# Kernel optimization log

Measured on AMD Instinct MI355X. Metric: run time of the kernel, lower is better.

The kernel has to match this reference:

```python
import jax, jax.numpy as jnp
import numpy as np

DIM = 1152
HEADS = 9
MID = 256
B, N = 8, 1024


def _conprefix(x, dw, db, uw, ub):
    # torch Linear: y = x @ W.T + b
    kv = jnp.tanh(x @ dw.T + db) @ uw.T + ub  # [B, N, 2*dim]
    q = jnp.zeros(kv.shape[:2] + (DIM,), kv.dtype)
    return jnp.concatenate([q, kv], axis=-1)  # [B, N, 3*dim]


def setup_inputs() -> dict:
    key = jax.random.key(0)
    ks = jax.random.split(key, 12)
    s = 0.02
    return {
        "x": jax.random.normal(ks[0], (B, N, DIM), dtype=jnp.float32),
        "Wqkv": jax.random.normal(ks[1], (3 * DIM, DIM), dtype=jnp.float32) * s,
        "Wproj": jax.random.normal(ks[2], (DIM, DIM), dtype=jnp.float32) * s,
        "bproj": jax.random.normal(ks[3], (DIM,), dtype=jnp.float32) * s,
        "down_w": jax.random.normal(ks[4], (MID, DIM), dtype=jnp.float32) * s,
        "down_b": jax.random.normal(ks[5], (MID,), dtype=jnp.float32) * s,
        "up_w": jax.random.normal(ks[6], (2 * DIM, MID), dtype=jnp.float32) * s,
        "up_b": jax.random.normal(ks[7], (2 * DIM,), dtype=jnp.float32) * s,
        "pdown_w": jax.random.normal(ks[8], (MID, DIM), dtype=jnp.float32) * s,
        "pdown_b": jax.random.normal(ks[9], (MID,), dtype=jnp.float32) * s,
        "pup_w": jax.random.normal(ks[10], (2 * DIM, MID), dtype=jnp.float32) * s,
        "pup_b": jax.random.normal(ks[11], (2 * DIM,), dtype=jnp.float32) * s,
        "task": 5,
    }


def reference(x, Wqkv, Wproj, bproj, down_w, down_b, up_w, up_b,
              pdown_w, pdown_b, pup_w, pup_b, task):
    b, n, c = x.shape
    hd = c // HEADS
    scale = hd ** (-0.5)
    qkv = x @ Wqkv.T  # [B, N, 3C] (qkv_bias=False)
    task_prefix_tensor = None
    if task <= 3:
        pass
    elif task == 4:
        qkv = qkv + _conprefix(x, down_w, down_b, up_w, up_b)
        task_prefix_tensor = down_w
    else:
        qkv = (qkv + _conprefix(x, pdown_w, pdown_b, pup_w, pup_b)
                   + _conprefix(x, down_w, down_b, up_w, up_b))
        task_prefix_tensor = down_w
    qkv = qkv.reshape(b, n, 3, HEADS, hd).transpose(2, 0, 3, 1, 4)  # [3,B,H,N,hd]
    q, k, v = qkv[0], qkv[1], qkv[2]
    attn = jax.nn.softmax(jnp.einsum('bhqd,bhkd->bhqk', q, k) * scale, axis=-1)
    out = jnp.einsum('bhqk,bhkd->bhqd', attn, v)  # [B,H,N,hd]
    out = out.transpose(0, 2, 1, 3).reshape(b, n, c)
    out = out @ Wproj.T + bproj
    return (out, task_prefix_tensor)
```

## Files before the change

### kernel.cpp

```cpp
#include <hip/hip_runtime.h>
#include <math.h>

namespace {

typedef unsigned short u16;
typedef __attribute__((ext_vector_type(8))) short short8;
typedef __attribute__((ext_vector_type(4))) float f32x4;
typedef __attribute__((ext_vector_type(16))) float f32x16;

constexpr int kDim   = 1152;
constexpr int kHeads = 9;
constexpr int kMid   = 256;
constexpr int kB     = 8;
constexpr int kN     = 1024;
constexpr int kM     = kB * kN;
constexpr int kQS    = 3584;
constexpr float kCexp  = 0.12753837360881433f;

__device__ __forceinline__ u16 f2bf(float f) {
    unsigned u = __builtin_bit_cast(unsigned, f);
    return (u16)((u + 0x7FFFu + ((u >> 16) & 1u)) >> 16);
}
__device__ __forceinline__ float bf2f(u16 h) {
    unsigned u = ((unsigned)h) << 16;
    return __builtin_bit_cast(float, u);
}

__device__ __forceinline__ void gload_lds16(const void* g, void* l) {
    __builtin_amdgcn_global_load_lds(
        (const __attribute__((address_space(1))) unsigned int*)g,
        (__attribute__((address_space(3))) unsigned int*)l,
        16, 0, 0);
}

__device__ __forceinline__ unsigned cvtpk(float a, float b) {
    unsigned r;
    asm volatile("v_cvt_pk_bf16_f32 %0, %1, %2" : "=v"(r) : "v"(a), "v"(b));
    return r;
}

__device__ __forceinline__ void halfswap(unsigned& x, unsigned& y, bool hihalf) {
    const unsigned xs = (unsigned)__shfl_xor((int)x, 32);
    const unsigned ys = (unsigned)__shfl_xor((int)y, 32);
    const unsigned nx = hihalf ? ys : x;
    const unsigned ny = hihalf ? y : xs;
    x = nx; y = ny;
}

__device__ __forceinline__ short8 build_pfrag(float p0, float p1, float p2, float p3,
                                              float p4, float p5, float p6, float p7,
                                              bool hihalf) {
    unsigned x1 = cvtpk(p0, p1), y1 = cvtpk(p4, p5);
    unsigned x2 = cvtpk(p2, p3), y2 = cvtpk(p6, p7);
    halfswap(x1, y1, hihalf);
    halfswap(x2, y2, hihalf);
    union { unsigned u[4]; short8 s; } pk;
    pk.u[0] = x1; pk.u[1] = x2; pk.u[2] = y1; pk.u[3] = y2;
    return pk.s;
}

constexpr int R0 = 2359296;
constexpr int R1 = R0 + 995328;
constexpr int R2 = R1 + 331776;
constexpr int R3 = R2 + 73728;
constexpr int R4 = R3 + 73728;
constexpr int R5 = R4 + 147456;
constexpr int R6 = R5 + 147456;
constexpr int R7 = R6 + 512;
constexpr int R8 = R7 + 2304;
constexpr int kQPart = 331776;
constexpr int kPrepGrid = R8 / 256;

__global__ __launch_bounds__(256)
void prep_all(const float* __restrict__ x, const float* __restrict__ Wqkv,
              const float* __restrict__ Wproj,
              const float* __restrict__ down_w, const float* __restrict__ pdown_w,
              const float* __restrict__ up_w, const float* __restrict__ pup_w,
              const float* __restrict__ down_b, const float* __restrict__ pdown_b,
              const float* __restrict__ up_b, const float* __restrict__ pup_b,
              const int* __restrict__ task,
              u16* __restrict__ xb, u16* __restrict__ wqkvb, u16* __restrict__ wprjb,
              u16* __restrict__ wdownb, u16* __restrict__ wupb,
              float* __restrict__ bd, float* __restrict__ bu)
{
    const int i = blockIdx.x * blockDim.x + threadIdx.x;
    auto cvt4s = [](const float* s, int j, float sc) {
        const float4 v = reinterpret_cast<const float4*>(s)[j];
        ushort4 o;
        o.x = f2bf(v.x * sc); o.y = f2bf(v.y * sc);
        o.z = f2bf(v.z * sc); o.w = f2bf(v.w * sc);
        return o;
    };
    if (i < R0) {
        reinterpret_cast<ushort4*>(xb)[i] = cvt4s(x, i, 1.f);
    } else if (i < R1) {
        const int j = i - R0;
        const float sc = (j < kQPart) ? kCexp : 1.f;
        reinterpret_cast<ushort4*>(wqkvb)[j] = cvt4s(Wqkv, j, sc);
    } else if (i < R2) {
        reinterpret_cast<ushort4*>(wprjb)[i - R1] = cvt4s(Wproj, i - R1, 1.f);
    } else if (i < R3) {
        reinterpret_cast<ushort4*>(wdownb)[i - R2] = cvt4s(down_w, i - R2, 1.f);
    } else if (i < R4) {
        reinterpret_cast<ushort4*>(wdownb)[73728 + (i - R3)] = cvt4s(pdown_w, i - R3, 1.f);
    } else if (i < R5) {
        const int j = i - R4, r = j >> 6, c = j & 63;
        reinterpret_cast<ushort4*>(wupb)[r * 128 + c] = cvt4s(up_w, j, 1.f);
    } else if (i < R6) {
        const int j = i - R5, r = j >> 6, c = j & 63;
        reinterpret_cast<ushort4*>(wupb)[r * 128 + 64 + c] = cvt4s(pup_w, j, 1.f);
    } else if (i < R7) {
        const int j = i - R6;
        bd[j] = (j < 256) ? down_b[j] : pdown_b[j - 256];
    } else {
        const int j = i - R7;
        bu[j] = up_b[j] + ((*task >= 5) ? pup_b[j] : 0.f);
    }
}

template<bool ACCUM, bool BIAS>
__global__ __launch_bounds__(512, 2)
void gemm8p(const u16* __restrict__ A, const u16* __restrict__ Bw,
            const float* __restrict__ bias, u16* __restrict__ C,
            int K, int lda, int ldb, int ldc)
{
    extern __shared__ char lds[];

    const int tid  = threadIdx.x;
    const int lane = tid & 63;
    const int wid  = tid >> 6;
    const int wm   = wid >> 2;
    const int wn   = wid & 3;
    const int bm   = blockIdx.x * 256;
    const int bn   = blockIdx.y * 256;
    const int l15  = lane & 15;
    const int kq   = lane >> 4;

    int srow[4], scol[4], sdst[4];
#pragma unroll
    for (int i = 0; i < 4; ++i) {
        const int id = i * 512 + tid;
        srow[i] = id >> 3;
        const int s = id & 7;
        scol[i] = (s ^ (srow[i] & 7)) * 8;
        sdst[i] = (i * 512 + wid * 64) * 16;
    }

    auto stage_pair = [&](int buf, int kt, int i) {
        const u16* ag = A  + (size_t)bm * lda + kt * 64;
        const u16* bg = Bw + (size_t)bn * ldb + kt * 64;
        gload_lds16(ag + (size_t)srow[i] * lda + scol[i], lds + buf * 32768 + sdst[i]);
        gload_lds16(bg + (size_t)srow[i] * ldb + scol[i], lds + 65536 + buf * 32768 + sdst[i]);
    };

    f32x4 acc[8][4] = {};
    const int nt = K >> 6;

#pragma unroll
    for (int i = 0; i < 4; ++i) stage_pair(0, 0, i);

    for (int t = 0; t < nt; ++t) {
        const char* Ab = lds + (t & 1) * 32768;
        const char* Bb = lds + 65536 + (t & 1) * 32768;
        const bool nxt = (t + 1 < nt);
        const int nb = (t + 1) & 1;

        short8 af[4], bf[4];

        auto rdA = [&](int mh, int ks) {
#pragma unroll
            for (int mi = 0; mi < 4; ++mi) {
                const int row = wm * 128 + mh * 64 + mi * 16 + l15;
                af[mi] = *reinterpret_cast<const short8*>(
                    Ab + row * 128 + (((ks * 4 + kq) ^ (row & 7)) * 16));
            }
        };
        auto rdB = [&](int ks) {
#pragma unroll
            for (int ni = 0; ni < 4; ++ni) {
                const int row = wn * 64 + ni * 16 + l15;
                bf[ni] = *reinterpret_cast<const short8*>(
                    Bb + row * 128 + (((ks * 4 + kq) ^ (row & 7)) * 16));
            }
        };
        auto mfma16 = [&](int mh) {
            asm volatile("s_waitcnt lgkmcnt(0)" ::: "memory");
            __builtin_amdgcn_sched_barrier(0);
            __builtin_amdgcn_s_setprio(1);
#pragma unroll
            for (int mi = 0; mi < 4; ++mi)
#pragma unroll
                for (int ni = 0; ni < 4; ++ni)
                    acc[mh * 4 + mi][ni] = __builtin_amdgcn_mfma_f32_16x16x32_bf16(
                        af[mi], bf[ni], acc[mh * 4 + mi][ni], 0, 0, 0);
            __builtin_amdgcn_s_setprio(0);
            asm volatile("" ::: "memory");
            __builtin_amdgcn_s_barrier();
            asm volatile("" ::: "memory");
        };

        if (nxt) { stage_pair(nb, t + 1, 0); stage_pair(nb, t + 1, 1); }
        if (nxt) asm volatile("s_waitcnt vmcnt(4)" ::: "memory");
        else     asm volatile("s_waitcnt vmcnt(0)" ::: "memory");
        __builtin_amdgcn_sched_barrier(0);
        __builtin_amdgcn_s_barrier();
        asm volatile("" ::: "memory");
        rdB(0); rdA(0, 0);
        mfma16(0);

        if (nxt) { stage_pair(nb, t + 1, 2); stage_pair(nb, t + 1, 3); }
        rdA(1, 0);
        mfma16(1);

        rdB(1); rdA(0, 1);
        mfma16(0);

        rdA(1, 1);
        mfma16(1);
    }

#pragma unroll
    for (int mg = 0; mg < 8; ++mg) {
#pragma unroll
        for (int ni = 0; ni < 4; ++ni) {
            const int col = bn + wn * 64 + ni * 16 + l15;
            const float bv = BIAS ? bias[col] : 0.f;
#pragma unroll
            for (int r = 0; r < 4; ++r) {
                const int row = bm + wm * 128 + mg * 16 + kq * 4 + r;
                float v = acc[mg][ni][r] + bv;
                u16* cp = C + (size_t)row * ldc + col;
                if (ACCUM) v += bf2f(*cp);
                *cp = f2bf(v);
            }
        }
    }
}

template<bool TANH, bool ACCUM, bool BIAS, bool OUT_BF16, bool KSEL>
__global__ __launch_bounds__(256)
void gemm_mfma(const u16* __restrict__ A, const u16* __restrict__ Bw,
               const float* __restrict__ bias, void* __restrict__ Cv,
               int K, int lda, int ldb, int ldc,
               const int* __restrict__ taskp, int mintask)
{
    if (taskp != nullptr && *taskp < mintask) return;
    if (KSEL && *taskp < 5) K = 256;

    __shared__ u16 As[2][128 * 64];
    __shared__ u16 Bs[2][128 * 64];

    const int tid  = threadIdx.x;
    const int lane = tid & 63;
    const int wv   = tid >> 6;
    const int wr   = (wv >> 1) * 64;
    const int wc   = (wv & 1) * 64;
    const int bm   = blockIdx.x * 128;
    const int bn   = blockIdx.y * 128;

    f32x4 acc[4][4] = {};

    const int srow = tid >> 3;
    const int sslt = tid & 7;

    auto stage = [&](int buf, int k0) {
        const u16* ab = A  + (size_t)bm * lda + k0;
        const u16* bb = Bw + (size_t)bn * ldb + k0;
#pragma unroll
        for (int i = 0; i < 4; ++i) {
            const int row = i * 32 + srow;
            gload_lds16(ab + (size_t)row * lda + sslt * 8,
                        (char*)&As[buf][0] + (i * 256 + (tid & 192)) * 16);
        }
#pragma unroll
        for (int i = 0; i < 4; ++i) {
            const int row = i * 32 + srow;
            gload_lds16(bb + (size_t)row * ldb + sslt * 8,
                        (char*)&Bs[buf][0] + (i * 256 + (tid & 192)) * 16);
        }
    };

    stage(0, 0);
    const int nk = K >> 6;
    for (int kt = 0; kt < nk; ++kt) {
        __syncthreads();
        if (kt + 1 < nk) stage((kt + 1) & 1, (kt + 1) * 64);
        const u16* as = &As[kt & 1][0];
        const u16* bs = &Bs[kt & 1][0];
#pragma unroll
        for (int ks = 0; ks < 2; ++ks) {
            short8 af[4], bf[4];
#pragma unroll
            for (int mi = 0; mi < 4; ++mi) {
                const int row = wr + mi * 16 + (lane & 15);
                af[mi] = *reinterpret_cast<const short8*>(as + row * 64 + ks * 32 + (lane >> 4) * 8);
            }
#pragma unroll
            for (int ni = 0; ni < 4; ++ni) {
                const int row = wc + ni * 16 + (lane & 15);
                bf[ni] = *reinterpret_cast<const short8*>(bs + row * 64 + ks * 32 + (lane >> 4) * 8);
            }
#pragma unroll
            for (int mi = 0; mi < 4; ++mi)
#pragma unroll
                for (int ni = 0; ni < 4; ++ni)
                    acc[mi][ni] = __builtin_amdgcn_mfma_f32_16x16x32_bf16(
                        af[mi], bf[ni], acc[mi][ni], 0, 0, 0);
        }
    }

#pragma unroll
    for (int mi = 0; mi < 4; ++mi) {
#pragma unroll
        for (int ni = 0; ni < 4; ++ni) {
            const int col = bn + wc + ni * 16 + (lane & 15);
            const float bv = BIAS ? bias[col] : 0.f;
#pragma unroll
            for (int r = 0; r < 4; ++r) {
                const int row = bm + wr + mi * 16 + (lane >> 4) * 4 + r;
                float v = acc[mi][ni][r] + bv;
                if (TANH) v = tanhf(v);
                if (OUT_BF16) {
                    u16* cp = (u16*)Cv + (size_t)row * ldc + col;
                    if (ACCUM) v += bf2f(*cp);
                    *cp = f2bf(v);
                } else {
                    float* cp = (float*)Cv + (size_t)row * ldc + col;
                    if (ACCUM) v += *cp;
                    *cp = v;
                }
            }
        }
    }
}

__global__ __launch_bounds__(256)
void transpose_v(const u16* __restrict__ qkv, u16* __restrict__ vt)
{
    __shared__ u16 t[64][136];
    const int bh = blockIdx.x, b = bh / kHeads, h = bh - b * kHeads;
    const int n0 = blockIdx.y * 64;
    const int tid = threadIdx.x;
#pragma unroll
    for (int it = 0; it < 4; ++it) {
        const int I = it * 256 + tid, tok = I >> 4, s = I & 15;
        *reinterpret_cast<short8*>(&t[tok][s * 8]) =
            *reinterpret_cast<const short8*>(
                qkv + (size_t)(b * kN + n0 + tok) * kQS + 2304 + h * 128 + s * 8);
    }
    __syncthreads();
#pragma unroll
    for (int it = 0; it < 8; ++it) {
        const int I = it * 256 + tid;
        const int d = I >> 4, tk = (I & 15) * 4;
        ushort4 v;
        v.x = t[tk + 0][d]; v.y = t[tk + 1][d];
        v.z = t[tk + 2][d]; v.w = t[tk + 3][d];
        *reinterpret_cast<ushort4*>(vt + (size_t)(bh * 128 + d) * kN + n0 + tk) = v;
    }
}

__global__ __launch_bounds__(256)
void attn_mfma(const u16* __restrict__ qkv, const u16* __restrict__ vt,
               u16* __restrict__ out)
{
    __shared__ u16 Ks[2][32 * 128];
    __shared__ u16 Vs[2][128 * 32];

    const int bh = blockIdx.x, b = bh / kHeads, h = bh - b * kHeads;
    const int tid = threadIdx.x, lane = tid & 63, wv = tid >> 6;
    const int lo5 = lane & 31;
    const bool hihalf = (lane >= 32);
    const int hi = hihalf ? 1 : 0;
    const int qh = wv >> 1;
    const int kh = wv & 1;
    const int q0 = blockIdx.y * 64 + qh * 32;

    const u16* qp = qkv + (size_t)(b * kN + q0 + lo5) * kQS + h * 128;
    short8 qf[8];
#pragma unroll
    for (int f = 0; f < 8; ++f)
        qf[f] = *reinterpret_cast<const short8*>(qp + f * 16 + hi * 8);

    int koff[2], voff[2];
#pragma unroll
    for (int j = 0; j < 2; ++j) {
        const int I = j * 256 + tid;
        const int tok = I >> 4, s = I & 15;
        koff[j] = tok * kQS + ((s ^ (tok & 7)) * 8);
        const int d = I >> 2, sv = I & 3;
        voff[j] = d * kN + ((sv ^ (d & 3)) * 8);
    }
    const u16* kbase = qkv + (size_t)b * kN * kQS + kDim + h * 128;
    const u16* vbase = vt + (size_t)bh * 128 * kN;

    f32x16 o[4] = {};
    float l = 0.f;

    for (int t = 0; t < 16; ++t) {
        __syncthreads();
#pragma unroll
        for (int hh = 0; hh < 2; ++hh) {
            const int kt = hh * 512 + t * 32;
#pragma unroll
            for (int j = 0; j < 2; ++j) {
                gload_lds16(kbase + (size_t)kt * kQS + koff[j],
                            (char*)&Ks[hh][0] + (j * 256 + wv * 64) * 16);
                gload_lds16(vbase + kt + voff[j],
                            (char*)&Vs[hh][0] + (j * 256 + wv * 64) * 16);
            }
        }
        __syncthreads();

        const char* ks = (const char*)&Ks[kh][0];
        const char* vs = (const char*)&Vs[kh][0];

        f32x16 s0 = {};
        __builtin_amdgcn_s_setprio(1);
#pragma unroll
        for (int f = 0; f < 8; ++f) {
            const short8 ka = *reinterpret_cast<const short8*>(
                ks + lo5 * 256 + (((f * 2 + hi) * 16) ^ ((lo5 & 7) << 4)));
            s0 = __builtin_amdgcn_mfma_f32_32x32x16_bf16(ka, qf[f], s0, 0, 0, 0);
        }
        __builtin_amdgcn_s_setprio(0);

        float rsum = 0.f;
#pragma unroll
        for (int r = 0; r < 16; ++r) { s0[r] = exp2f(s0[r]); rsum += s0[r]; }
        rsum += __shfl_xor(rsum, 32);
        l += rsum;

        short8 pf[2];
        pf[0] = build_pfrag(s0[0], s0[1], s0[2], s0[3], s0[4], s0[5], s0[6], s0[7], hihalf);
        pf[1] = build_pfrag(s0[8], s0[9], s0[10], s0[11], s0[12], s0[13], s0[14], s0[15], hihalf);

        __builtin_amdgcn_s_setprio(1);
#pragma unroll
        for (int dt = 0; dt < 4; ++dt) {
            const int drow = dt * 32 + lo5;
#pragma unroll
            for (int c = 0; c < 2; ++c) {
                const short8 va = *reinterpret_cast<const short8*>(
                    vs + drow * 64 + (((c * 2 + hi) * 16) ^ ((drow & 3) << 4)));
                o[dt] = __builtin_amdgcn_mfma_f32_32x32x16_bf16(va, pf[c], o[dt], 0, 0, 0);
            }
        }
        __builtin_amdgcn_s_setprio(0);
    }

    __syncthreads();
    char* exch = (char*)&Ks[0][0];
    float* ls  = (float*)&Vs[0][0];
    if (kh == 1) {
#pragma unroll
        for (int dt = 0; dt < 4; ++dt) {
#pragma unroll
            for (int rg = 0; rg < 4; ++rg) {
                const int kb = (dt * 4 + rg) * 8;
                ushort4 w;
                w.x = f2bf(o[dt][rg * 4 + 0]);
                w.y = f2bf(o[dt][rg * 4 + 1]);
                w.z = f2bf(o[dt][rg * 4 + 2]);
                w.w = f2bf(o[dt][rg * 4 + 3]);
                *reinterpret_cast<ushort4*>(
                    exch + qh * 8192 + lane * 128 + (kb ^ ((lane & 7) << 3))) = w;
            }
        }
        if (!hihalf) ls[qh * 32 + lo5] = l;
    }
    __syncthreads();
    if (kh == 0) {
        const float inv = 1.f / (l + ls[qh * 32 + lo5]);
        u16* op = out + (size_t)(b * kN + q0 + lo5) * kDim + h * 128;
#pragma unroll
        for (int dt = 0; dt < 4; ++dt) {
#pragma unroll
            for (int rg = 0; rg < 4; ++rg) {
                const int kb = (dt * 4 + rg) * 8;
                const ushort4 pv = *reinterpret_cast<const ushort4*>(
                    exch + qh * 8192 + lane * 128 + (kb ^ ((lane & 7) << 3)));
                const int d0 = dt * 32 + rg * 8 + hi * 4;
                ushort4 v;
                v.x = f2bf((o[dt][rg * 4 + 0] + bf2f(pv.x)) * inv);
                v.y = f2bf((o[dt][rg * 4 + 1] + bf2f(pv.y)) * inv);
                v.z = f2bf((o[dt][rg * 4 + 2] + bf2f(pv.z)) * inv);
                v.w = f2bf((o[dt][rg * 4 + 3] + bf2f(pv.w)) * inv);
                *reinterpret_cast<ushort4*>(op + d0) = v;
            }
        }
    }
}

}

extern "C" void kernel_launch(void* const* d_in, const int* in_sizes, int n_in,
                              void* d_out, int out_size, void* d_ws, size_t ws_size,
                              hipStream_t stream)
{
    const float* x       = (const float*)d_in[0];
    const float* Wqkv    = (const float*)d_in[1];
    const float* Wproj   = (const float*)d_in[2];
    const float* bproj   = (const float*)d_in[3];
    const float* down_w  = (const float*)d_in[4];
    const float* down_b  = (const float*)d_in[5];
    const float* up_w    = (const float*)d_in[6];
    const float* up_b    = (const float*)d_in[7];
    const float* pdown_w = (const float*)d_in[8];
    const float* pdown_b = (const float*)d_in[9];
    const float* pup_w   = (const float*)d_in[10];
    const float* pup_b   = (const float*)d_in[11];
    const int*   task    = (const int*)d_in[12];

    u16* xb_vt  = (u16*)d_ws;
    u16* wqkvb  = xb_vt  + (size_t)kM * kDim;
    u16* wprjb  = wqkvb  + (size_t)kQS * kDim;
    u16* wdownb = wprjb  + (size_t)kDim * kDim;
    u16* wupb   = wdownb + (size_t)512 * kDim;
    u16* h12    = wupb   + (size_t)2304 * 512;
    u16* qkvb   = h12    + (size_t)kM * 512;
    u16* aob    = qkvb   + (size_t)kM * kQS;
    float* bd   = (float*)(aob + (size_t)kM * kDim);
    float* bu   = bd + 512;
    float* out  = (float*)d_out;
    u16* xb = xb_vt;
    u16* vt = xb_vt;

    prep_all<<<kPrepGrid, 256, 0, stream>>>(
        x, Wqkv, Wproj, down_w, pdown_w, up_w, pup_w,
        down_b, pdown_b, up_b, pup_b, task,
        xb, wqkvb, wprjb, wdownb, wupb, bd, bu);

    hipFuncSetAttribute(reinterpret_cast<const void*>(&gemm8p<false, false>),
                        hipFuncAttributeMaxDynamicSharedMemorySize, 131072);

    gemm_mfma<true, false, true, true, false><<<dim3(kM / 128, 4), 256, 0, stream>>>(
        xb, wdownb, bd, h12, kDim, kDim, kDim, 512, nullptr, 0);
    gemm8p<false, false><<<dim3(kM / 256, kQS / 256), 512, 131072, stream>>>(
        xb, wqkvb, nullptr, qkvb, kDim, kDim, kDim, kQS);
    gemm_mfma<false, true, true, true, true><<<dim3(kM / 128, 18), 256, 0, stream>>>(
        h12, wupb, bu, qkvb + kDim, 512, 512, 512, kQS, task, 4);

    transpose_v<<<dim3(kB * kHeads, kN / 64), 256, 0, stream>>>(qkvb, vt);

    attn_mfma<<<dim3(kB * kHeads, kN / 64), 256, 0, stream>>>(qkvb, vt, aob);

    gemm_mfma<false, false, true, false, false><<<dim3(kM / 128, 9), 256, 0, stream>>>(
        aob, wprjb, bproj, out, kDim, kDim, kDim, kDim, nullptr, 0);

    hipMemcpyAsync(out + (size_t)kM * kDim, down_w,
                   (size_t)kMid * kDim * sizeof(float),
                   hipMemcpyDeviceToDevice, stream);
}
```

Baseline: 330.4 us.

## Halve GEMM K-tile to cut LDS use; restage attention K/V tiles

The QKV GEMM kernel drops its K-step from 64 to 32. That halves dynamic LDS from 128KB to 64KB, and the launch bounds now ask for 4 blocks per CU instead of 2, trading twice as many barriers and stages for higher occupancy. The attention kernel now loads one 64-row K tile and a 128x64 V tile per iteration into single unified LDS buffers with 8-way XOR swizzles, in place of two separate 32-wide halves. That changes the load mapping and the bank-conflict pattern. The request for 4 blocks of 512 threads may force register spilling given the 128 accumulator floats per thread.

```diff
diff --git a/kernel.cpp b/kernel.cpp
--- a/kernel.cpp
+++ b/kernel.cpp
@@ -119,8 +119,8 @@
 }
 
 template<bool ACCUM, bool BIAS>
-__global__ __launch_bounds__(512, 2)
-void gemm8p(const u16* __restrict__ A, const u16* __restrict__ Bw,
+__global__ __launch_bounds__(512, 4)
+void gemm2b(const u16* __restrict__ A, const u16* __restrict__ Bw,
             const float* __restrict__ bias, u16* __restrict__ C,
             int K, int lda, int ldb, int ldc)
 {
@@ -136,51 +136,50 @@
     const int l15  = lane & 15;
     const int kq   = lane >> 4;
 
-    int srow[4], scol[4], sdst[4];
-#pragma unroll
-    for (int i = 0; i < 4; ++i) {
+    int srow[2], scol[2], sdst[2];
+#pragma unroll
+    for (int i = 0; i < 2; ++i) {
         const int id = i * 512 + tid;
-        srow[i] = id >> 3;
-        const int s = id & 7;
-        scol[i] = (s ^ (srow[i] & 7)) * 8;
+        srow[i] = id >> 2;
+        const int s = id & 3;
+        scol[i] = (s ^ (srow[i] & 3)) * 8;
         sdst[i] = (i * 512 + wid * 64) * 16;
     }
 
-    auto stage_pair = [&](int buf, int kt, int i) {
-        const u16* ag = A  + (size_t)bm * lda + kt * 64;
-        const u16* bg = Bw + (size_t)bn * ldb + kt * 64;
-        gload_lds16(ag + (size_t)srow[i] * lda + scol[i], lds + buf * 32768 + sdst[i]);
-        gload_lds16(bg + (size_t)srow[i] * ldb + scol[i], lds + 65536 + buf * 32768 + sdst[i]);
+    auto stage = [&](int buf, int kt) {
+        const u16* ag = A  + (size_t)bm * lda + kt * 32;
+        const u16* bg = Bw + (size_t)bn * ldb + kt * 32;
+#pragma unroll
+        for (int i = 0; i < 2; ++i) {
+            gload_lds16(ag + (size_t)srow[i] * lda + scol[i], lds + buf * 16384 + sdst[i]);
+            gload_lds16(bg + (size_t)srow[i] * ldb + scol[i], lds + 32768 + buf * 16384 + sdst[i]);
+        }
     };
 
     f32x4 acc[8][4] = {};
-    const int nt = K >> 6;
-
-#pragma unroll
-    for (int i = 0; i < 4; ++i) stage_pair(0, 0, i);
+    const int nt = K >> 5;
+
+    stage(0, 0);
 
     for (int t = 0; t < nt; ++t) {
-        const char* Ab = lds + (t & 1) * 32768;
-        const char* Bb = lds + 65536 + (t & 1) * 32768;
+        const char* Ab = lds + (t & 1) * 16384;
+        const char* Bb = lds + 32768 + (t & 1) * 16384;
         const bool nxt = (t + 1 < nt);
-        const int nb = (t + 1) & 1;
+
+        if (nxt) stage((t + 1) & 1, t + 1);
+        if (nxt) asm volatile("s_waitcnt vmcnt(4)" ::: "memory");
+        else     asm volatile("s_waitcnt vmcnt(0)" ::: "memory");
+        __builtin_amdgcn_sched_barrier(0);
+        __builtin_amdgcn_s_barrier();
+        asm volatile("" ::: "memory");
 
         short8 af[4], bf[4];
-
-        auto rdA = [&](int mh, int ks) {
+        auto rdA = [&](int mh) {
 #pragma unroll
             for (int mi = 0; mi < 4; ++mi) {
                 const int row = wm * 128 + mh * 64 + mi * 16 + l15;
                 af[mi] = *reinterpret_cast<const short8*>(
-                    Ab + row * 128 + (((ks * 4 + kq) ^ (row & 7)) * 16));
-            }
-        };
-        auto rdB = [&](int ks) {
-#pragma unroll
-            for (int ni = 0; ni < 4; ++ni) {
-                const int row = wn * 64 + ni * 16 + l15;
-                bf[ni] = *reinterpret_cast<const short8*>(
-                    Bb + row * 128 + (((ks * 4 + kq) ^ (row & 7)) * 16));
+                    Ab + row * 64 + ((kq ^ (row & 3)) * 16));
             }
         };
         auto mfma16 = [&](int mh) {
@@ -199,23 +198,15 @@
             asm volatile("" ::: "memory");
         };
 
-        if (nxt) { stage_pair(nb, t + 1, 0); stage_pair(nb, t + 1, 1); }
-        if (nxt) asm volatile("s_waitcnt vmcnt(4)" ::: "memory");
-        else     asm volatile("s_waitcnt vmcnt(0)" ::: "memory");
-        __builtin_amdgcn_sched_barrier(0);
-        __builtin_amdgcn_s_barrier();
-        asm volatile("" ::: "memory");
-        rdB(0); rdA(0, 0);
+#pragma unroll
+        for (int ni = 0; ni < 4; ++ni) {
+            const int row = wn * 64 + ni * 16 + l15;
+            bf[ni] = *reinterpret_cast<const short8*>(
+                Bb + row * 64 + ((kq ^ (row & 3)) * 16));
+        }
+        rdA(0);
         mfma16(0);
-
-        if (nxt) { stage_pair(nb, t + 1, 2); stage_pair(nb, t + 1, 3); }
-        rdA(1, 0);
-        mfma16(1);
-
-        rdB(1); rdA(0, 1);
-        mfma16(0);
-
-        rdA(1, 1);
+        rdA(1);
         mfma16(1);
     }
 
@@ -364,8 +355,8 @@
 void attn_mfma(const u16* __restrict__ qkv, const u16* __restrict__ vt,
                u16* __restrict__ out)
 {
-    __shared__ u16 Ks[2][32 * 128];
-    __shared__ u16 Vs[2][128 * 32];
+    __shared__ u16 Ks[64 * 128];
+    __shared__ u16 Vs[128 * 64];
 
     const int bh = blockIdx.x, b = bh / kHeads, h = bh - b * kHeads;
     const int tid = threadIdx.x, lane = tid & 63, wv = tid >> 6;
@@ -382,14 +373,16 @@
     for (int f = 0; f < 8; ++f)
         qf[f] = *reinterpret_cast<const short8*>(qp + f * 16 + hi * 8);
 
-    int koff[2], voff[2];
-#pragma unroll
-    for (int j = 0; j < 2; ++j) {
+    int koff[4], voff[4];
+#pragma unroll
+    for (int j = 0; j < 4; ++j) {
         const int I = j * 256 + tid;
-        const int tok = I >> 4, s = I & 15;
-        koff[j] = tok * kQS + ((s ^ (tok & 7)) * 8);
-        const int d = I >> 2, sv = I & 3;
-        voff[j] = d * kN + ((sv ^ (d & 3)) * 8);
+        const int row = I >> 4, s = I & 15;
+        const int tokK = (row >> 5) * 512 + (row & 31);
+        koff[j] = tokK * kQS + ((s ^ (row & 7)) * 8);
+        const int d = I >> 3, u = I & 7;
+        const int cs = u ^ (d & 7);
+        voff[j] = d * kN + ((cs >> 2) * 512 + (cs & 3) * 8);
     }
     const u16* kbase = qkv + (size_t)b * kN * kQS + kDim + h * 128;
     const u16* vbase = vt + (size_t)bh * 128 * kN;
@@ -400,27 +393,22 @@
     for (int t = 0; t < 16; ++t) {
         __syncthreads();
 #pragma unroll
-        for (int hh = 0; hh < 2; ++hh) {
-            const int kt = hh * 512 + t * 32;
-#pragma unroll
-            for (int j = 0; j < 2; ++j) {
-                gload_lds16(kbase + (size_t)kt * kQS + koff[j],
-                            (char*)&Ks[hh][0] + (j * 256 + wv * 64) * 16);
-                gload_lds16(vbase + kt + voff[j],
-                            (char*)&Vs[hh][0] + (j * 256 + wv * 64) * 16);
-            }
-        }
+        for (int j = 0; j < 4; ++j)
+            gload_lds16(kbase + (size_t)(t * 32) * kQS + koff[j],
+                        (char*)Ks + (j * 256 + wv * 64) * 16);
+#pragma unroll
+        for (int j = 0; j < 4; ++j)
+            gload_lds16(vbase + t * 32 + voff[j],
+                        (char*)Vs + (j * 256 + wv * 64) * 16);
         __syncthreads();
 
-        const char* ks = (const char*)&Ks[kh][0];
-        const char* vs = (const char*)&Vs[kh][0];
-
+        const int rr = kh * 32 + lo5;
         f32x16 s0 = {};
         __builtin_amdgcn_s_setprio(1);
 #pragma unroll
         for (int f = 0; f < 8; ++f) {
             const short8 ka = *reinterpret_cast<const short8*>(
-                ks + lo5 * 256 + (((f * 2 + hi) * 16) ^ ((lo5 & 7) << 4)));
+                (const char*)Ks + rr * 256 + (((f * 2 + hi) * 16) ^ ((rr & 7) << 4)));
             s0 = __builtin_amdgcn_mfma_f32_32x32x16_bf16(ka, qf[f], s0, 0, 0, 0);
         }
         __builtin_amdgcn_s_setprio(0);
@@ -442,7 +430,8 @@
 #pragma unroll
             for (int c = 0; c < 2; ++c) {
                 const short8 va = *reinterpret_cast<const short8*>(
-                    vs + drow * 64 + (((c * 2 + hi) * 16) ^ ((drow & 3) << 4)));
+                    (const char*)Vs + drow * 128 +
+                    (((kh * 4 + c * 2 + hi) * 16) ^ ((drow & 7) << 4)));
                 o[dt] = __builtin_amdgcn_mfma_f32_32x32x16_bf16(va, pf[c], o[dt], 0, 0, 0);
             }
         }
@@ -450,8 +439,8 @@
     }
 
     __syncthreads();
-    char* exch = (char*)&Ks[0][0];
-    float* ls  = (float*)&Vs[0][0];
+    char* exch = (char*)Ks;
+    float* ls  = (float*)Vs;
     if (kh == 1) {
 #pragma unroll
         for (int dt = 0; dt < 4; ++dt) {
@@ -531,12 +520,12 @@
         down_b, pdown_b, up_b, pup_b, task,
         xb, wqkvb, wprjb, wdownb, wupb, bd, bu);
 
-    hipFuncSetAttribute(reinterpret_cast<const void*>(&gemm8p<false, false>),
-                        hipFuncAttributeMaxDynamicSharedMemorySize, 131072);
+    hipFuncSetAttribute(reinterpret_cast<const void*>(&gemm2b<false, false>),
+                        hipFuncAttributeMaxDynamicSharedMemorySize, 65536);
 
     gemm_mfma<true, false, true, true, false><<<dim3(kM / 128, 4), 256, 0, stream>>>(
         xb, wdownb, bd, h12, kDim, kDim, kDim, 512, nullptr, 0);
-    gemm8p<false, false><<<dim3(kM / 256, kQS / 256), 512, 131072, stream>>>(
+    gemm2b<false, false><<<dim3(kM / 256, kQS / 256), 512, 65536, stream>>>(
         xb, wqkvb, nullptr, qkvb, kDim, kDim, kDim, kQS);
     gemm_mfma<false, true, true, true, true><<<dim3(kM / 128, 18), 256, 0, stream>>>(
         h12, wupb, bu, qkvb + kDim, 512, 512, 512, kQS, task, 4);
```

Result: slower. 719.9 us (+117.9%).

## Fuse V transpose into up-projection epilogue and register-prefetch K/V tiles in attention

Applied to the files above, without the earlier changes.

Removes the standalone transpose_v kernel by having the prefix up-projection GEMM epilogue write the V columns directly into the transposed vt buffer. When the task gate is off, the kernel still runs with a zero gate so that vt is produced. The attention kernel replaces direct global-to-LDS loads with a register-staged prefetch of the next K/V tile, overlapping global loads with MFMA compute. The trade-offs are extra register pressure and strided 8-byte stores in the GEMM epilogue.

```diff
diff --git a/kernel.cpp b/kernel.cpp
--- a/kernel.cpp
+++ b/kernel.cpp
@@ -237,14 +237,19 @@
     }
 }
 
-template<bool TANH, bool ACCUM, bool BIAS, bool OUT_BF16, bool KSEL>
+template<bool TANH, bool ACCUM, bool BIAS, bool OUT_BF16, bool KSEL, bool VT>
 __global__ __launch_bounds__(256)
 void gemm_mfma(const u16* __restrict__ A, const u16* __restrict__ Bw,
                const float* __restrict__ bias, void* __restrict__ Cv,
+               u16* __restrict__ vt,
                int K, int lda, int ldb, int ldc,
                const int* __restrict__ taskp, int mintask)
 {
-    if (taskp != nullptr && *taskp < mintask) return;
+    float gate = 1.f;
+    if (taskp != nullptr && *taskp < mintask) {
+        if (!VT) return;
+        gate = 0.f;
+    }
     if (KSEL && *taskp < 5) K = 256;
 
     __shared__ u16 As[2][128 * 64];
@@ -315,48 +320,34 @@
         for (int ni = 0; ni < 4; ++ni) {
             const int col = bn + wc + ni * 16 + (lane & 15);
             const float bv = BIAS ? bias[col] : 0.f;
+            ushort4 tv;
 #pragma unroll
             for (int r = 0; r < 4; ++r) {
                 const int row = bm + wr + mi * 16 + (lane >> 4) * 4 + r;
-                float v = acc[mi][ni][r] + bv;
+                float v = gate * (acc[mi][ni][r] + bv);
                 if (TANH) v = tanhf(v);
                 if (OUT_BF16) {
                     u16* cp = (u16*)Cv + (size_t)row * ldc + col;
                     if (ACCUM) v += bf2f(*cp);
-                    *cp = f2bf(v);
+                    const u16 bb = f2bf(v);
+                    *cp = bb;
+                    if (VT) (&tv.x)[r] = bb;
                 } else {
                     float* cp = (float*)Cv + (size_t)row * ldc + col;
                     if (ACCUM) v += *cp;
                     *cp = v;
                 }
             }
-        }
-    }
-}
-
-__global__ __launch_bounds__(256)
-void transpose_v(const u16* __restrict__ qkv, u16* __restrict__ vt)
-{
-    __shared__ u16 t[64][136];
-    const int bh = blockIdx.x, b = bh / kHeads, h = bh - b * kHeads;
-    const int n0 = blockIdx.y * 64;
-    const int tid = threadIdx.x;
-#pragma unroll
-    for (int it = 0; it < 4; ++it) {
-        const int I = it * 256 + tid, tok = I >> 4, s = I & 15;
-        *reinterpret_cast<short8*>(&t[tok][s * 8]) =
-            *reinterpret_cast<const short8*>(
-                qkv + (size_t)(b * kN + n0 + tok) * kQS + 2304 + h * 128 + s * 8);
-    }
-    __syncthreads();
-#pragma unroll
-    for (int it = 0; it < 8; ++it) {
-        const int I = it * 256 + tid;
-        const int d = I >> 4, tk = (I & 15) * 4;
-        ushort4 v;
-        v.x = t[tk + 0][d]; v.y = t[tk + 1][d];
-        v.z = t[tk + 2][d]; v.w = t[tk + 3][d];
-        *reinterpret_cast<ushort4*>(vt + (size_t)(bh * 128 + d) * kN + n0 + tk) = v;
+            if (VT && col >= 1152) {
+                const int hh = (col - 1152) >> 7;
+                const int d  = (col - 1152) & 127;
+                const int row0 = bm + wr + mi * 16 + (lane >> 4) * 4;
+                const int bb_  = row0 >> 10;
+                const int tok  = row0 & 1023;
+                *reinterpret_cast<ushort4*>(
+                    vt + ((size_t)(bb_ * kHeads + hh) * 128 + d) * kN + tok) = tv;
+            }
+        }
     }
 }
 
@@ -394,23 +385,38 @@
     const u16* kbase = qkv + (size_t)b * kN * kQS + kDim + h * 128;
     const u16* vbase = vt + (size_t)bh * 128 * kN;
 
+    uint4 kr0, kr1, kr2, kr3, vr0, vr1, vr2, vr3;
+    auto ldregs = [&](int t) {
+        const int kt0 = t * 32, kt1 = 512 + t * 32;
+        kr0 = *reinterpret_cast<const uint4*>(kbase + (size_t)kt0 * kQS + koff[0]);
+        kr1 = *reinterpret_cast<const uint4*>(kbase + (size_t)kt0 * kQS + koff[1]);
+        kr2 = *reinterpret_cast<const uint4*>(kbase + (size_t)kt1 * kQS + koff[0]);
+        kr3 = *reinterpret_cast<const uint4*>(kbase + (size_t)kt1 * kQS + koff[1]);
+        vr0 = *reinterpret_cast<const uint4*>(vbase + kt0 + voff[0]);
+        vr1 = *reinterpret_cast<const uint4*>(vbase + kt0 + voff[1]);
+        vr2 = *reinterpret_cast<const uint4*>(vbase + kt1 + voff[0]);
+        vr3 = *reinterpret_cast<const uint4*>(vbase + kt1 + voff[1]);
+    };
+    auto stlds = [&]() {
+        *reinterpret_cast<uint4*>((char*)&Ks[0][0] + (0 * 256 + wv * 64 + lane) * 16) = kr0;
+        *reinterpret_cast<uint4*>((char*)&Ks[0][0] + (1 * 256 + wv * 64 + lane) * 16) = kr1;
+        *reinterpret_cast<uint4*>((char*)&Ks[1][0] + (0 * 256 + wv * 64 + lane) * 16) = kr2;
+        *reinterpret_cast<uint4*>((char*)&Ks[1][0] + (1 * 256 + wv * 64 + lane) * 16) = kr3;
+        *reinterpret_cast<uint4*>((char*)&Vs[0][0] + (0 * 256 + wv * 64 + lane) * 16) = vr0;
+        *reinterpret_cast<uint4*>((char*)&Vs[0][0] + (1 * 256 + wv * 64 + lane) * 16) = vr1;
+        *reinterpret_cast<uint4*>((char*)&Vs[1][0] + (0 * 256 + wv * 64 + lane) * 16) = vr2;
+        *reinterpret_cast<uint4*>((char*)&Vs[1][0] + (1 * 256 + wv * 64 + lane) * 16) = vr3;
+    };
+
     f32x16 o[4] = {};
     float l = 0.f;
 
+    ldregs(0);
+    stlds();
+    __syncthreads();
+
     for (int t = 0; t < 16; ++t) {
-        __syncthreads();
-#pragma unroll
-        for (int hh = 0; hh < 2; ++hh) {
-            const int kt = hh * 512 + t * 32;
-#pragma unroll
-            for (int j = 0; j < 2; ++j) {
-                gload_lds16(kbase + (size_t)kt * kQS + koff[j],
-                            (char*)&Ks[hh][0] + (j * 256 + wv * 64) * 16);
-                gload_lds16(vbase + kt + voff[j],
-                            (char*)&Vs[hh][0] + (j * 256 + wv * 64) * 16);
-            }
-        }
-        __syncthreads();
+        if (t + 1 < 16) ldregs(t + 1);
 
         const char* ks = (const char*)&Ks[kh][0];
         const char* vs = (const char*)&Vs[kh][0];
@@ -447,9 +453,12 @@
             }
         }
         __builtin_amdgcn_s_setprio(0);
-    }
-
-    __syncthreads();
+
+        __syncthreads();
+        if (t + 1 < 16) stlds();
+        __syncthreads();
+    }
+
     char* exch = (char*)&Ks[0][0];
     float* ls  = (float*)&Vs[0][0];
     if (kh == 1) {
@@ -534,19 +543,17 @@
     hipFuncSetAttribute(reinterpret_cast<const void*>(&gemm8p<false, false>),
                         hipFuncAttributeMaxDynamicSharedMemorySize, 131072);
 
-    gemm_mfma<true, false, true, true, false><<<dim3(kM / 128, 4), 256, 0, stream>>>(
-        xb, wdownb, bd, h12, kDim, kDim, kDim, 512, nullptr, 0);
+    gemm_mfma<true, false, true, true, false, false><<<dim3(kM / 128, 4), 256, 0, stream>>>(
+        xb, wdownb, bd, h12, nullptr, kDim, kDim, kDim, 512, nullptr, 0);
     gemm8p<false, false><<<dim3(kM / 256, kQS / 256), 512, 131072, stream>>>(
         xb, wqkvb, nullptr, qkvb, kDim, kDim, kDim, kQS);
-    gemm_mfma<false, true, true, true, true><<<dim3(kM / 128, 18), 256, 0, stream>>>(
-        h12, wupb, bu, qkvb + kDim, 512, 512, 512, kQS, task, 4);
-
-    transpose_v<<<dim3(kB * kHeads, kN / 64), 256, 0, stream>>>(qkvb, vt);
+    gemm_mfma<false, true, true, true, true, true><<<dim3(kM / 128, 18), 256, 0, stream>>>(
+        h12, wupb, bu, qkvb + kDim, vt, 512, 512, 512, kQS, task, 4);
 
     attn_mfma<<<dim3(kB * kHeads, kN / 64), 256, 0, stream>>>(qkvb, vt, aob);
 
-    gemm_mfma<false, false, true, false, false><<<dim3(kM / 128, 9), 256, 0, stream>>>(
-        aob, wprjb, bproj, out, kDim, kDim, kDim, kDim, nullptr, 0);
+    gemm_mfma<false, false, true, false, false, false><<<dim3(kM / 128, 9), 256, 0, stream>>>(
+        aob, wprjb, bproj, out, nullptr, kDim, kDim, kDim, kDim, nullptr, 0);
 
     hipMemcpyAsync(out + (size_t)kM * kDim, down_w,
                    (size_t)kMid * kDim * sizeof(float),
```

Result: slower. 337.9 us (+2.2%).

## Fuse up-projection GEMM into QKV GEMM via K-concatenated operands

Applied to the files above, without the earlier changes.

Concatenates x and the tanh down-projection output along K into one activation buffer, and builds a matching concatenated weight matrix (Wqkv rows padded with zeros, up/pup weights placed in the extra K columns for the KV rows). The QKV GEMM then computes qkv plus both prefix contributions in a single pass, with K chosen at runtime from task and a fused bias vector. This removes the separate up-projection GEMM and its read-modify-write of the bf16 qkv buffer. In exchange the main GEMM does extra K work across all N columns, including the zero-padded Q block, and the prep kernel writes a larger strided layout.

```diff
diff --git a/kernel.cpp b/kernel.cpp
--- a/kernel.cpp
+++ b/kernel.cpp
@@ -15,6 +15,7 @@
 constexpr int kN     = 1024;
 constexpr int kM     = kB * kN;
 constexpr int kQS    = 3584;
+constexpr int kKC    = 1664;
 constexpr float kCexp  = 0.12753837360881433f;
 
 __device__ __forceinline__ u16 f2bf(float f) {
@@ -59,17 +60,18 @@
     return pk.s;
 }
 
-constexpr int R0 = 2359296;
-constexpr int R1 = R0 + 995328;
-constexpr int R2 = R1 + 331776;
-constexpr int R3 = R2 + 73728;
-constexpr int R4 = R3 + 73728;
-constexpr int R5 = R4 + 147456;
-constexpr int R6 = R5 + 147456;
-constexpr int R7 = R6 + 512;
-constexpr int R8 = R7 + 2304;
+constexpr int P0 = 2359296;
+constexpr int P1 = P0 + 995328;
+constexpr int P2 = P1 + 147456;
+constexpr int P3 = P2 + 147456;
+constexpr int P4 = P3 + 147456;
+constexpr int P5 = P4 + 331776;
+constexpr int P6 = P5 + 73728;
+constexpr int P7 = P6 + 73728;
+constexpr int P8 = P7 + 512;
+constexpr int P9 = P8 + 3584;
 constexpr int kQPart = 331776;
-constexpr int kPrepGrid = R8 / 256;
+constexpr int kPrepGrid = P9 / 256;
 
 __global__ __launch_bounds__(256)
 void prep_all(const float* __restrict__ x, const float* __restrict__ Wqkv,
@@ -79,9 +81,9 @@
               const float* __restrict__ down_b, const float* __restrict__ pdown_b,
               const float* __restrict__ up_b, const float* __restrict__ pup_b,
               const int* __restrict__ task,
-              u16* __restrict__ xb, u16* __restrict__ wqkvb, u16* __restrict__ wprjb,
-              u16* __restrict__ wdownb, u16* __restrict__ wupb,
-              float* __restrict__ bd, float* __restrict__ bu)
+              u16* __restrict__ acat, u16* __restrict__ bcat,
+              u16* __restrict__ wprjb, u16* __restrict__ wdownb,
+              float* __restrict__ bd, float* __restrict__ bq)
 {
     const int i = blockIdx.x * blockDim.x + threadIdx.x;
     auto cvt4s = [](const float* s, int j, float sc) {
@@ -91,40 +93,53 @@
         o.z = f2bf(v.z * sc); o.w = f2bf(v.w * sc);
         return o;
     };
-    if (i < R0) {
-        reinterpret_cast<ushort4*>(xb)[i] = cvt4s(x, i, 1.f);
-    } else if (i < R1) {
-        const int j = i - R0;
+    if (i < P0) {
+        const int r = i / 288, c = i - r * 288;
+        reinterpret_cast<ushort4*>(acat)[r * 416 + c] = cvt4s(x, i, 1.f);
+    } else if (i < P1) {
+        const int j = i - P0;
         const float sc = (j < kQPart) ? kCexp : 1.f;
-        reinterpret_cast<ushort4*>(wqkvb)[j] = cvt4s(Wqkv, j, sc);
-    } else if (i < R2) {
-        reinterpret_cast<ushort4*>(wprjb)[i - R1] = cvt4s(Wproj, i - R1, 1.f);
-    } else if (i < R3) {
-        reinterpret_cast<ushort4*>(wdownb)[i - R2] = cvt4s(down_w, i - R2, 1.f);
-    } else if (i < R4) {
-        reinterpret_cast<ushort4*>(wdownb)[73728 + (i - R3)] = cvt4s(pdown_w, i - R3, 1.f);
-    } else if (i < R5) {
-        const int j = i - R4, r = j >> 6, c = j & 63;
-        reinterpret_cast<ushort4*>(wupb)[r * 128 + c] = cvt4s(up_w, j, 1.f);
-    } else if (i < R6) {
-        const int j = i - R5, r = j >> 6, c = j & 63;
-        reinterpret_cast<ushort4*>(wupb)[r * 128 + 64 + c] = cvt4s(pup_w, j, 1.f);
-    } else if (i < R7) {
-        const int j = i - R6;
+        const int r = j / 288, c = j - r * 288;
+        reinterpret_cast<ushort4*>(bcat)[r * 416 + c] = cvt4s(Wqkv, j, sc);
+    } else if (i < P2) {
+        const int j = i - P1, r = j >> 7, c = j & 127;
+        reinterpret_cast<ushort4*>(bcat)[r * 416 + 288 + c] = ushort4{0, 0, 0, 0};
+    } else if (i < P3) {
+        const int j = i - P2, r = j >> 6, c = j & 63;
+        reinterpret_cast<ushort4*>(bcat)[(1152 + r) * 416 + 288 + c] = cvt4s(up_w, j, 1.f);
+    } else if (i < P4) {
+        const int j = i - P3, r = j >> 6, c = j & 63;
+        reinterpret_cast<ushort4*>(bcat)[(1152 + r) * 416 + 352 + c] = cvt4s(pup_w, j, 1.f);
+    } else if (i < P5) {
+        reinterpret_cast<ushort4*>(wprjb)[i - P4] = cvt4s(Wproj, i - P4, 1.f);
+    } else if (i < P6) {
+        reinterpret_cast<ushort4*>(wdownb)[i - P5] = cvt4s(down_w, i - P5, 1.f);
+    } else if (i < P7) {
+        reinterpret_cast<ushort4*>(wdownb)[73728 + (i - P6)] = cvt4s(pdown_w, i - P6, 1.f);
+    } else if (i < P8) {
+        const int j = i - P7;
         bd[j] = (j < 256) ? down_b[j] : pdown_b[j - 256];
     } else {
-        const int j = i - R7;
-        bu[j] = up_b[j] + ((*task >= 5) ? pup_b[j] : 0.f);
-    }
-}
-
-template<bool ACCUM, bool BIAS>
+        const int j = i - P8;
+        float v = 0.f;
+        if (j >= 1152 && j < 3456 && *task >= 4) {
+            v = up_b[j - 1152];
+            if (*task >= 5) v += pup_b[j - 1152];
+        }
+        bq[j] = v;
+    }
+}
+
 __global__ __launch_bounds__(512, 2)
 void gemm8p(const u16* __restrict__ A, const u16* __restrict__ Bw,
             const float* __restrict__ bias, u16* __restrict__ C,
-            int K, int lda, int ldb, int ldc)
+            const int* __restrict__ taskp)
 {
     extern __shared__ char lds[];
+
+    const int tk = *taskp;
+    const int K = (tk >= 5) ? 1664 : ((tk >= 4) ? 1408 : 1152);
+    const int lda = kKC, ldb = kKC, ldc = kQS;
 
     const int tid  = threadIdx.x;
     const int lane = tid & 63;
@@ -224,29 +239,22 @@
 #pragma unroll
         for (int ni = 0; ni < 4; ++ni) {
             const int col = bn + wn * 64 + ni * 16 + l15;
-            const float bv = BIAS ? bias[col] : 0.f;
+            const float bv = bias[col];
 #pragma unroll
             for (int r = 0; r < 4; ++r) {
                 const int row = bm + wm * 128 + mg * 16 + kq * 4 + r;
-                float v = acc[mg][ni][r] + bv;
-                u16* cp = C + (size_t)row * ldc + col;
-                if (ACCUM) v += bf2f(*cp);
-                *cp = f2bf(v);
-            }
-        }
-    }
-}
-
-template<bool TANH, bool ACCUM, bool BIAS, bool OUT_BF16, bool KSEL>
+                C[(size_t)row * ldc + col] = f2bf(acc[mg][ni][r] + bv);
+            }
+        }
+    }
+}
+
+template<bool TANH, bool BIAS, bool OUT_BF16>
 __global__ __launch_bounds__(256)
 void gemm_mfma(const u16* __restrict__ A, const u16* __restrict__ Bw,
                const float* __restrict__ bias, void* __restrict__ Cv,
-               int K, int lda, int ldb, int ldc,
-               const int* __restrict__ taskp, int mintask)
+               int K, int lda, int ldb, int ldc)
 {
-    if (taskp != nullptr && *taskp < mintask) return;
-    if (KSEL && *taskp < 5) K = 256;
-
     __shared__ u16 As[2][128 * 64];
     __shared__ u16 Bs[2][128 * 64];
 
@@ -321,13 +329,9 @@
                 float v = acc[mi][ni][r] + bv;
                 if (TANH) v = tanhf(v);
                 if (OUT_BF16) {
-                    u16* cp = (u16*)Cv + (size_t)row * ldc + col;
-                    if (ACCUM) v += bf2f(*cp);
-                    *cp = f2bf(v);
+                    ((u16*)Cv)[(size_t)row * ldc + col] = f2bf(v);
                 } else {
-                    float* cp = (float*)Cv + (size_t)row * ldc + col;
-                    if (ACCUM) v += *cp;
-                    *cp = v;
+                    ((float*)Cv)[(size_t)row * ldc + col] = v;
                 }
             }
         }
@@ -512,41 +516,37 @@
     const float* pup_b   = (const float*)d_in[11];
     const int*   task    = (const int*)d_in[12];
 
-    u16* xb_vt  = (u16*)d_ws;
-    u16* wqkvb  = xb_vt  + (size_t)kM * kDim;
-    u16* wprjb  = wqkvb  + (size_t)kQS * kDim;
+    u16* acat   = (u16*)d_ws;
+    u16* bcat   = acat   + (size_t)kM * kKC;
+    u16* wprjb  = bcat   + (size_t)kQS * kKC;
     u16* wdownb = wprjb  + (size_t)kDim * kDim;
-    u16* wupb   = wdownb + (size_t)512 * kDim;
-    u16* h12    = wupb   + (size_t)2304 * 512;
-    u16* qkvb   = h12    + (size_t)kM * 512;
+    u16* qkvb   = wdownb + (size_t)512 * kDim;
     u16* aob    = qkvb   + (size_t)kM * kQS;
     float* bd   = (float*)(aob + (size_t)kM * kDim);
-    float* bu   = bd + 512;
+    float* bq   = bd + 512;
     float* out  = (float*)d_out;
-    u16* xb = xb_vt;
-    u16* vt = xb_vt;
+    u16* vt = acat;
 
     prep_all<<<kPrepGrid, 256, 0, stream>>>(
         x, Wqkv, Wproj, down_w, pdown_w, up_w, pup_w,
         down_b, pdown_b, up_b, pup_b, task,
-        xb, wqkvb, wprjb, wdownb, wupb, bd, bu);
-
-    hipFuncSetAttribute(reinterpret_cast<const void*>(&gemm8p<false, false>),
+        acat, bcat, wprjb, wdownb, bd, bq);
+
+    hipFuncSetAttribute(reinterpret_cast<const void*>(&gemm8p),
                         hipFuncAttributeMaxDynamicSharedMemorySize, 131072);
 
-    gemm_mfma<true, false, true, true, false><<<dim3(kM / 128, 4), 256, 0, stream>>>(
-        xb, wdownb, bd, h12, kDim, kDim, kDim, 512, nullptr, 0);
-    gemm8p<false, false><<<dim3(kM / 256, kQS / 256), 512, 131072, stream>>>(
-        xb, wqkvb, nullptr, qkvb, kDim, kDim, kDim, kQS);
-    gemm_mfma<false, true, true, true, true><<<dim3(kM / 128, 18), 256, 0, stream>>>(
-        h12, wupb, bu, qkvb + kDim, 512, 512, 512, kQS, task, 4);
+    gemm_mfma<true, true, true><<<dim3(kM / 128, 4), 256, 0, stream>>>(
+        acat, wdownb, bd, acat + kDim, kDim, kKC, kDim, kKC);
+
+    gemm8p<<<dim3(kM / 256, kQS / 256), 512, 131072, stream>>>(
+        acat, bcat, bq, qkvb, task);
 
     transpose_v<<<dim3(kB * kHeads, kN / 64), 256, 0, stream>>>(qkvb, vt);
 
     attn_mfma<<<dim3(kB * kHeads, kN / 64), 256, 0, stream>>>(qkvb, vt, aob);
 
-    gemm_mfma<false, false, true, false, false><<<dim3(kM / 128, 9), 256, 0, stream>>>(
-        aob, wprjb, bproj, out, kDim, kDim, kDim, kDim, nullptr, 0);
+    gemm_mfma<false, true, false><<<dim3(kM / 128, 9), 256, 0, stream>>>(
+        aob, wprjb, bproj, out, kDim, kDim, kDim, kDim);
 
     hipMemcpyAsync(out + (size_t)kM * kDim, down_w,
                    (size_t)kMid * kDim * sizeof(float),
```

Result: faster. 280.6 us (-15.1%).
